# Performance work log

Measured on AMD Instinct MI355X. Metric: run time of the kernel, lower is better.

## Reference

```python
import jax, jax.numpy as jnp
import numpy as np

B, S, H = 4, 4096, 1024
E, K, DE, DS = 8, 2, 128, 512  # n_routed_experts, top_k, routed hidden, shared hidden


def setup_inputs() -> dict:
    key = jax.random.key(0)
    ks = jax.random.split(key, 10)
    sc = 0.02
    return {
        "x": jax.random.normal(ks[0], (B, S, H), dtype=jnp.float32),
        "Wg": jax.random.normal(ks[1], (E, H), dtype=jnp.float32) * sc,
        "W1": jax.random.normal(ks[2], (E, DE, H), dtype=jnp.float32) * sc,
        "b1": jnp.zeros((E, DE), dtype=jnp.float32),
        "W2": jax.random.normal(ks[3], (E, H, DE), dtype=jnp.float32) * sc,
        "b2": jnp.zeros((E, H), dtype=jnp.float32),
        "Ws1": jax.random.normal(ks[4], (DS, H), dtype=jnp.float32) * sc,
        "bs1": jnp.zeros((DS,), dtype=jnp.float32),
        "Ws2": jax.random.normal(ks[5], (H, DS), dtype=jnp.float32) * sc,
        "bs2": jnp.zeros((H,), dtype=jnp.float32),
    }


def reference(x, Wg, W1, b1, W2, b2, Ws1, bs1, Ws2, bs2):
    # FFNMoE forward, eval mode (dropout = identity, aux loss inactive).
    xf = x.reshape(-1, H)  # [T, H]
    # --- MOEGate: softmax scoring + top-k + normalized weights ---
    logits = xf @ Wg.T                         # [T, E]
    scores = jax.nn.softmax(logits, axis=-1)
    topk_w, topk_idx = jax.lax.top_k(scores, K)  # [T, K]
    topk_w = topk_w / (jnp.sum(topk_w, axis=-1, keepdims=True) + 1e-20)
    # Dense per-(token, expert) combine weight (topk indices are distinct).
    w = jnp.sum(jax.nn.one_hot(topk_idx, E, dtype=xf.dtype) * topk_w[..., None], axis=1)  # [T, E]
    # --- Routed experts: fc1 -> relu -> fc2, weighted scatter-combine ---
    h1 = jax.nn.relu(jnp.einsum('th,efh->tef', xf, W1) + b1)       # [T, E, DE]
    y = jnp.einsum('tef,ehf,te->th', h1, W2, w) + w @ b2           # [T, H]
    # --- Shared expert ---
    sh = jax.nn.relu(xf @ Ws1.T + bs1) @ Ws2.T + bs2               # [T, H]
    return (y + sh).reshape(x.shape)
```

## Files before the change

### kernel.cpp

```cpp
#include <hip/hip_runtime.h>
#include <cstdint>

#define TTOK 16384
#define HD   1024
#define NE   8
#define NDE  128
#define NDS  512
#define NC1  1536
#define KC2  1536
#define NPAIR 28
#define MAXT  160
#define PREPB 3080
#define GATEB 1024
#define NH    768

typedef float  f32x4  __attribute__((ext_vector_type(4)));
typedef __bf16 bf16x8 __attribute__((ext_vector_type(8)));

__device__ __forceinline__ unsigned short f2bf(float f) {
  unsigned int u = __float_as_uint(f);
  u += 0x7fffu + ((u >> 16) & 1u);
  return (unsigned short)(u >> 16);
}

__device__ __forceinline__ void gl2lds16(const void* gp, void* lp) {
  void* g0 = const_cast<void*>(gp);
  __builtin_amdgcn_global_load_lds((__attribute__((address_space(1))) void*)g0,
                                   (__attribute__((address_space(3))) void*)lp,
                                   16, 0, 0);
}

__global__ __launch_bounds__(256) void prep_gate(
    const float* __restrict__ x, const float* __restrict__ Wg,
    const float* __restrict__ W1, const float* __restrict__ Ws1,
    const float* __restrict__ W2, const float* __restrict__ Ws2,
    const float* __restrict__ b1, const float* __restrict__ bs1,
    unsigned short* __restrict__ W1cat, unsigned short* __restrict__ W2cat,
    float* __restrict__ bias1, unsigned short* __restrict__ xbf,
    float2* __restrict__ wpair, int* __restrict__ pid) {
  if (blockIdx.x < PREPB) {
    const int total = NC1 * HD + HD * KC2 + NC1;
    for (int idx = blockIdx.x * 256 + threadIdx.x; idx < total; idx += PREPB * 256) {
      if (idx < NC1 * HD) {
        int r = idx >> 10, k = idx & 1023;
        float v = (r < 1024) ? W1[idx] : Ws1[(size_t)(r - 1024) * HD + k];
        W1cat[idx] = f2bf(v);
      } else if (idx < NC1 * HD + HD * KC2) {
        int i2 = idx - NC1 * HD;
        int h = i2 / KC2;
        int j = i2 - h * KC2;
        float v = (j < 1024) ? W2[(size_t)((j >> 7) * HD + h) * NDE + (j & 127)]
                             : Ws2[(size_t)h * NDS + (j - 1024)];
        W2cat[i2] = f2bf(v);
      } else {
        int r = idx - (NC1 * HD + HD * KC2);
        bias1[r] = (r < 1024) ? b1[r] : bs1[r - 1024];
      }
    }
    return;
  }
  __shared__ float part[16 * 8 * 64];
  __shared__ float lgs[128];

  const int tid  = threadIdx.x;
  const int lane = tid & 63;
  const int wv   = tid >> 6;
  const int g    = blockIdx.x - PREPB;
  const int tokb = g * 16 + wv * 4;

  const float* xr = x + (size_t)tokb * HD + lane * 16;
  float4 xv[4][4];
#pragma unroll
  for (int t = 0; t < 4; ++t)
#pragma unroll
    for (int c = 0; c < 4; ++c)
      xv[t][c] = ((const float4*)(xr + (size_t)t * HD))[c];

#pragma unroll
  for (int t = 0; t < 4; ++t) {
    unsigned short* xo = xbf + (size_t)(tokb + t) * HD + lane * 16;
    union { unsigned short us[8]; uint4 v; } pk;
    pk.us[0] = f2bf(xv[t][0].x); pk.us[1] = f2bf(xv[t][0].y);
    pk.us[2] = f2bf(xv[t][0].z); pk.us[3] = f2bf(xv[t][0].w);
    pk.us[4] = f2bf(xv[t][1].x); pk.us[5] = f2bf(xv[t][1].y);
    pk.us[6] = f2bf(xv[t][1].z); pk.us[7] = f2bf(xv[t][1].w);
    ((uint4*)xo)[0] = pk.v;
    pk.us[0] = f2bf(xv[t][2].x); pk.us[1] = f2bf(xv[t][2].y);
    pk.us[2] = f2bf(xv[t][2].z); pk.us[3] = f2bf(xv[t][2].w);
    pk.us[4] = f2bf(xv[t][3].x); pk.us[5] = f2bf(xv[t][3].y);
    pk.us[6] = f2bf(xv[t][3].z); pk.us[7] = f2bf(xv[t][3].w);
    ((uint4*)xo)[1] = pk.v;
  }

  float p[4][8];
#pragma unroll
  for (int t = 0; t < 4; ++t)
#pragma unroll
    for (int e = 0; e < 8; ++e) p[t][e] = 0.f;
#pragma unroll
  for (int e = 0; e < 8; ++e) {
    const float4* wr = (const float4*)(Wg + (size_t)e * HD + lane * 16);
    float4 w0 = wr[0], w1 = wr[1], w2 = wr[2], w3 = wr[3];
#pragma unroll
    for (int t = 0; t < 4; ++t) {
      p[t][e] = w0.x * xv[t][0].x + w0.y * xv[t][0].y + w0.z * xv[t][0].z + w0.w * xv[t][0].w +
                w1.x * xv[t][1].x + w1.y * xv[t][1].y + w1.z * xv[t][1].z + w1.w * xv[t][1].w +
                w2.x * xv[t][2].x + w2.y * xv[t][2].y + w2.z * xv[t][2].z + w2.w * xv[t][2].w +
                w3.x * xv[t][3].x + w3.y * xv[t][3].y + w3.z * xv[t][3].z + w3.w * xv[t][3].w;
    }
  }
#pragma unroll
  for (int t = 0; t < 4; ++t)
#pragma unroll
    for (int e = 0; e < 8; ++e) {
      int j = (wv * 4 + t) * 8 + e;
      part[j * 64 + ((lane + 4 * j) & 63)] = p[t][e];
    }
  __syncthreads();

  if (tid < 128) {
    float s = 0.f;
#pragma unroll
    for (int m = 0; m < 16; ++m) {
      int kk = (4 * m + 4 * tid) & 63;
      float4 v = *(const float4*)&part[tid * 64 + kk];
      s += v.x + v.y + v.z + v.w;
    }
    lgs[tid] = s;
  }
  __syncthreads();

  if (tid < 16) {
    float lg[8];
#pragma unroll
    for (int e = 0; e < 8; ++e) lg[e] = lgs[tid * 8 + e];
    int i1 = 0; float m1 = lg[0];
#pragma unroll
    for (int e = 1; e < 8; ++e) { if (lg[e] > m1) { m1 = lg[e]; i1 = e; } }
    int i2 = -1; float m2 = -3.4e38f;
#pragma unroll
    for (int e = 0; e < 8; ++e) { if (e != i1 && lg[e] > m2) { m2 = lg[e]; i2 = e; } }
    float Z = 0.f;
#pragma unroll
    for (int e = 0; e < 8; ++e) Z += expf(lg[e] - m1);
    float s1 = 1.f / Z;
    float s2 = expf(m2 - m1) / Z;
    float dn = s1 + s2 + 1e-20f;
    float w1 = s1 / dn, w2 = s2 / dn;
    int ef, es; float wf, wsx;
    if (i1 < i2) { ef = i1; es = i2; wf = w1; wsx = w2; }
    else         { ef = i2; es = i1; wf = w2; wsx = w1; }
    int pq = ef * 7 - (ef * (ef - 1)) / 2 + (es - ef - 1);
    int t = g * 16 + tid;
    wpair[t] = make_float2(wf, wsx);
    pid[t] = pq;
  }
}

__global__ __launch_bounds__(256) void route_scan(const int* __restrict__ pid,
                                                  int* __restrict__ perm,
                                                  int4* __restrict__ tiletab,
                                                  int* __restrict__ ntct) {
  __shared__ int hist[256 * 29];
  __shared__ int totals[NPAIR];
  __shared__ int spre[256];
  const int p   = blockIdx.x;
  const int tid = threadIdx.x;
#pragma unroll
  for (int q = 0; q < 29; ++q) hist[tid * 29 + q] = 0;
  __syncthreads();
  for (int k = 0; k < 64; ++k) {
    int q = pid[tid + (k << 8)];
    hist[tid * 29 + q]++;
  }
  __syncthreads();
  if (tid < NPAIR) {
    int s = 0;
    for (int i = 0; i < 256; ++i) s += hist[i * 29 + tid];
    totals[tid] = s;
  }
  __syncthreads();
  const int mycnt = hist[tid * 29 + p];
  spre[tid] = mycnt;
  __syncthreads();
  for (int d = 1; d < 256; d <<= 1) {
    int add = (tid >= d) ? spre[tid - d] : 0;
    __syncthreads();
    spre[tid] += add;
    __syncthreads();
  }
  int estart = 0, tstart = 0;
  for (int q = 0; q < p; ++q) { estart += totals[q]; tstart += (totals[q] + 127) >> 7; }
  const int cp = totals[p];
  const int nt = (cp + 127) >> 7;
  if (p == NPAIR - 1 && tid == 0) ntct[0] = tstart + nt;
  for (int k = tid; k < nt; k += 256) {
    int4 e;
    e.x = p;
    e.y = estart + (k << 7);
    e.z = min(128, cp - (k << 7));
    e.w = (tstart + k) << 7;
    tiletab[tstart + k] = e;
  }
  int wr = estart + spre[tid] - mycnt;
  for (int k = 0; k < 64; ++k) {
    int t = tid + (k << 8);
    if (pid[t] == p) perm[wr++] = t;
  }
}

__global__ __launch_bounds__(256) void moe_fc1(const unsigned short* __restrict__ xbf,
                                               const unsigned short* __restrict__ W1cat,
                                               const int* __restrict__ perm,
                                               const float2* __restrict__ wpair,
                                               const float* __restrict__ bias1,
                                               const int4* __restrict__ tiletab,
                                               const int* __restrict__ ntct,
                                               unsigned short* __restrict__ Hbuf) {
  const int L   = blockIdx.x;
  const int xcd = L & 7;
  const int s   = L >> 3;
  const int mg  = s / 6;
  const int nn  = s - mg * 6;
  const int mt  = xcd + (mg << 3);
  if (mt >= ntct[0]) return;
  const int4 tt = tiletab[mt];
  const int eoff = tt.y, valid = tt.z, hbase = tt.w;
  int ef = 0, rem = tt.x;
  while (rem >= 7 - ef) { rem -= 7 - ef; ef++; }
  const int es = ef + 1 + rem;
  const int brow = (nn == 0) ? ef * 128 : (nn == 1) ? es * 128 : 1024 + ((nn - 2) << 7);

  __shared__ __align__(16) unsigned short As[128 * 64];
  __shared__ __align__(16) unsigned short Bs[128 * 64];

  const int tid  = threadIdx.x;
  const int lane = tid & 63;
  const int wv   = tid >> 6;
  const int wm   = wv >> 1;
  const int wn   = wv & 1;
  const int r16  = lane & 15;
  const int quad = lane >> 4;

  const unsigned short* gA[4];
  const unsigned short* gB[4];
  unsigned short* lA[4];
  unsigned short* lB[4];
#pragma unroll
  for (int i = 0; i < 4; ++i) {
    int idx = i * 256 + tid;
    int row = idx >> 3;
    int cc  = idx & 7;
    int kc  = cc ^ (row & 7);
    int tok = perm[eoff + min(row, valid - 1)];
    gA[i] = xbf + (size_t)tok * HD + kc * 8;
    gB[i] = W1cat + (size_t)(brow + row) * HD + kc * 8;
    lA[i] = As + idx * 8;
    lB[i] = Bs + idx * 8;
  }

  int aoff[4], boff[4];
#pragma unroll
  for (int i = 0; i < 4; ++i) {
    int ra = wm * 64 + i * 16 + r16;
    aoff[i] = ra * 64 + ((quad ^ (ra & 7)) << 3);
    int rb = wn * 64 + i * 16 + r16;
    boff[i] = rb * 64 + ((quad ^ (rb & 7)) << 3);
  }

  f32x4 acc[4][4];
#pragma unroll
  for (int i = 0; i < 4; ++i)
#pragma unroll
    for (int j = 0; j < 4; ++j) acc[i][j] = (f32x4){0.f, 0.f, 0.f, 0.f};

  for (int kt = 0; kt < 16; ++kt) {
    const int ko = kt << 6;
#pragma unroll
    for (int i = 0; i < 4; ++i) gl2lds16(gA[i] + ko, lA[i]);
#pragma unroll
    for (int i = 0; i < 4; ++i) gl2lds16(gB[i] + ko, lB[i]);
    __syncthreads();
#pragma unroll
    for (int g = 0; g < 2; ++g) {
      const int gx = g << 5;
      bf16x8 av[4], bv[4];
#pragma unroll
      for (int i = 0; i < 4; ++i) av[i] = *(const bf16x8*)(As + (aoff[i] ^ gx));
#pragma unroll
      for (int j = 0; j < 4; ++j) bv[j] = *(const bf16x8*)(Bs + (boff[j] ^ gx));
#pragma unroll
      for (int i = 0; i < 4; ++i)
#pragma unroll
        for (int j = 0; j < 4; ++j)
          acc[i][j] = __builtin_amdgcn_mfma_f32_16x16x32_bf16(av[i], bv[j], acc[i][j], 0, 0, 0);
    }
    __syncthreads();
  }

  float* wl = (float*)As;
  if (tid < 128) {
    int tok = perm[eoff + min(tid, valid - 1)];
    float sc = 1.0f;
    if (nn == 0) sc = wpair[tok].x;
    else if (nn == 1) sc = wpair[tok].y;
    wl[tid] = sc;
  }
  __syncthreads();
#pragma unroll
  for (int j = 0; j < 4; ++j) {
    const int cin = wn * 64 + j * 16 + r16;
    const float bz = bias1[brow + cin];
#pragma unroll
    for (int i = 0; i < 4; ++i) {
#pragma unroll
      for (int r = 0; r < 4; ++r) {
        const int lrow = wm * 64 + i * 16 + quad * 4 + r;
        float v = fmaxf(acc[i][j][r] + bz, 0.f) * wl[lrow];
        Hbuf[(size_t)(hbase + lrow) * NH + nn * 128 + cin] = f2bf(v);
      }
    }
  }
}

__global__ __launch_bounds__(256) void moe_fc2(const unsigned short* __restrict__ Hbuf,
                                               const unsigned short* __restrict__ W2cat,
                                               const int* __restrict__ perm,
                                               const float2* __restrict__ wpair,
                                               const float* __restrict__ b2,
                                               const float* __restrict__ bs2,
                                               const int4* __restrict__ tiletab,
                                               const int* __restrict__ ntct,
                                               float* __restrict__ out) {
  const int L   = blockIdx.x;
  const int xcd = L & 7;
  const int s   = L >> 3;
  const int mg  = s >> 3;
  const int nn  = s & 7;
  const int mt  = xcd + (mg << 3);
  if (mt >= ntct[0]) return;
  const int4 tt = tiletab[mt];
  const int eoff = tt.y, valid = tt.z, hbase = tt.w;
  int ef = 0, rem = tt.x;
  while (rem >= 7 - ef) { rem -= 7 - ef; ef++; }
  const int es = ef + 1 + rem;
  const int tileN = nn << 7;

  __shared__ __align__(16) unsigned short As[128 * 64];
  __shared__ __align__(16) unsigned short Bs[128 * 64];

  const int tid  = threadIdx.x;
  const int lane = tid & 63;
  const int wv   = tid >> 6;
  const int wm   = wv >> 1;
  const int wn   = wv & 1;
  const int r16  = lane & 15;
  const int quad = lane >> 4;

  const unsigned short* gA[4];
  const unsigned short* gB[4];
  unsigned short* lA[4];
  unsigned short* lB[4];
#pragma unroll
  for (int i = 0; i < 4; ++i) {
    int idx = i * 256 + tid;
    int row = idx >> 3;
    int cc  = idx & 7;
    int kc  = cc ^ (row & 7);
    gA[i] = Hbuf + (size_t)(hbase + row) * NH + kc * 8;
    gB[i] = W2cat + (size_t)(tileN + row) * KC2 + kc * 8;
    lA[i] = As + idx * 8;
    lB[i] = Bs + idx * 8;
  }

  int aoff[4], boff[4];
#pragma unroll
  for (int i = 0; i < 4; ++i) {
    int ra = wm * 64 + i * 16 + r16;
    aoff[i] = ra * 64 + ((quad ^ (ra & 7)) << 3);
    int rb = wn * 64 + i * 16 + r16;
    boff[i] = rb * 64 + ((quad ^ (rb & 7)) << 3);
  }

  f32x4 acc[4][4];
#pragma unroll
  for (int i = 0; i < 4; ++i)
#pragma unroll
    for (int j = 0; j < 4; ++j) acc[i][j] = (f32x4){0.f, 0.f, 0.f, 0.f};

  for (int kt = 0; kt < 12; ++kt) {
    const int koA = kt << 6;
    const int koB = (kt < 2) ? ef * 128 + (kt << 6)
                 : (kt < 4) ? es * 128 + ((kt - 2) << 6)
                            : 1024 + ((kt - 4) << 6);
#pragma unroll
    for (int i = 0; i < 4; ++i) gl2lds16(gA[i] + koA, lA[i]);
#pragma unroll
    for (int i = 0; i < 4; ++i) gl2lds16(gB[i] + koB, lB[i]);
    __syncthreads();
#pragma unroll
    for (int g = 0; g < 2; ++g) {
      const int gx = g << 5;
      bf16x8 av[4], bv[4];
#pragma unroll
      for (int i = 0; i < 4; ++i) av[i] = *(const bf16x8*)(As + (aoff[i] ^ gx));
#pragma unroll
      for (int j = 0; j < 4; ++j) bv[j] = *(const bf16x8*)(Bs + (boff[j] ^ gx));
#pragma unroll
      for (int i = 0; i < 4; ++i)
#pragma unroll
        for (int j = 0; j < 4; ++j)
          acc[i][j] = __builtin_amdgcn_mfma_f32_16x16x32_bf16(av[i], bv[j], acc[i][j], 0, 0, 0);
    }
    __syncthreads();
  }

  float2* wl2 = (float2*)As;
  int* tokl   = (int*)Bs;
  if (tid < 128) {
    int tokc = perm[eoff + min(tid, valid - 1)];
    tokl[tid] = (tid < valid) ? tokc : -1;
    wl2[tid] = wpair[tokc];
  }
  __syncthreads();
  float bsc[4], b2a[4], b2b[4];
#pragma unroll
  for (int j = 0; j < 4; ++j) {
    const int col = tileN + wn * 64 + j * 16 + r16;
    bsc[j] = bs2[col];
    b2a[j] = b2[(size_t)ef * HD + col];
    b2b[j] = b2[(size_t)es * HD + col];
  }
#pragma unroll
  for (int i = 0; i < 4; ++i) {
#pragma unroll
    for (int r = 0; r < 4; ++r) {
      const int lrow = wm * 64 + i * 16 + quad * 4 + r;
      const int tok = tokl[lrow];
      if (tok < 0) continue;
      const float2 w = wl2[lrow];
#pragma unroll
      for (int j = 0; j < 4; ++j) {
        const int col = tileN + wn * 64 + j * 16 + r16;
        out[(size_t)tok * HD + col] = acc[i][j][r] + bsc[j] + w.x * b2a[j] + w.y * b2b[j];
      }
    }
  }
}

extern "C" void kernel_launch(void* const* d_in, const int* in_sizes, int n_in,
                              void* d_out, int out_size, void* d_ws, size_t ws_size,
                              hipStream_t stream) {
  const float* x   = (const float*)d_in[0];
  const float* Wg  = (const float*)d_in[1];
  const float* W1  = (const float*)d_in[2];
  const float* b1  = (const float*)d_in[3];
  const float* W2  = (const float*)d_in[4];
  const float* b2  = (const float*)d_in[5];
  const float* Ws1 = (const float*)d_in[6];
  const float* bs1 = (const float*)d_in[7];
  const float* Ws2 = (const float*)d_in[8];
  const float* bs2 = (const float*)d_in[9];

  char* ws = (char*)d_ws;
  size_t off = 0;
  unsigned short* xbf   = (unsigned short*)(ws + off); off += (size_t)TTOK * HD * 2;
  unsigned short* Hbuf  = (unsigned short*)(ws + off); off += (size_t)MAXT * 128 * NH * 2;
  unsigned short* W1cat = (unsigned short*)(ws + off); off += (size_t)NC1 * HD * 2;
  unsigned short* W2cat = (unsigned short*)(ws + off); off += (size_t)HD * KC2 * 2;
  float* bias1          = (float*)(ws + off);          off += (size_t)NC1 * 4;
  float2* wpair         = (float2*)(ws + off);         off += (size_t)TTOK * 8;
  int* pid              = (int*)(ws + off);            off += (size_t)TTOK * 4;
  int* perm             = (int*)(ws + off);            off += (size_t)TTOK * 4;
  int4* tiletab         = (int4*)(ws + off);           off += (size_t)MAXT * 16;
  int* ntct             = (int*)(ws + off);            off += 16;

  prep_gate<<<PREPB + GATEB, 256, 0, stream>>>(x, Wg, W1, Ws1, W2, Ws2, b1, bs1,
                                               W1cat, W2cat, bias1, xbf, wpair, pid);
  route_scan<<<NPAIR, 256, 0, stream>>>(pid, perm, tiletab, ntct);
  moe_fc1<<<8 * 20 * 6, 256, 0, stream>>>(xbf, W1cat, perm, wpair, bias1, tiletab, ntct, Hbuf);
  moe_fc2<<<8 * 20 * 8, 256, 0, stream>>>(Hbuf, W2cat, perm, wpair, b2, bs2, tiletab, ntct,
                                          (float*)d_out);
}
```

Measured before the change: 250.1 us.

## Restructure expert GEMMs to one 128x128 tile per wave with double-buffered async loads

Both expert GEMM kernels now give each wavefront a whole 128x128 output tile, with private LDS double buffers filled by global_load_lds and vmcnt waits. This removes block-wide __syncthreads and overlaps the next K-slice load with the MFMA work, using smaller K steps of 32. The cost is a 256-register accumulator per wave and occupancy forced to one block per CU. Per-wave B-tile reuse is lost, and fewer blocks are launched.

```diff
diff --git a/kernel.cpp b/kernel.cpp
--- a/kernel.cpp
+++ b/kernel.cpp
@@ -29,6 +29,10 @@
                                    (__attribute__((address_space(3))) void*)lp,
                                    16, 0, 0);
 }
+
+#define VM16 asm volatile("s_waitcnt vmcnt(16)" ::: "memory")
+#define VM0  asm volatile("s_waitcnt vmcnt(0)"  ::: "memory")
+#define LGFENCE do { asm volatile("s_waitcnt lgkmcnt(0)" ::: "memory"); } while (0)
 
 __global__ __launch_bounds__(256) void prep_gate(
     const float* __restrict__ x, const float* __restrict__ Wg,
@@ -209,241 +213,212 @@
   }
 }
 
-__global__ __launch_bounds__(256) void moe_fc1(const unsigned short* __restrict__ xbf,
-                                               const unsigned short* __restrict__ W1cat,
-                                               const int* __restrict__ perm,
-                                               const float2* __restrict__ wpair,
-                                               const float* __restrict__ bias1,
-                                               const int4* __restrict__ tiletab,
-                                               const int* __restrict__ ntct,
-                                               unsigned short* __restrict__ Hbuf) {
-  const int L   = blockIdx.x;
-  const int xcd = L & 7;
-  const int s   = L >> 3;
-  const int mg  = s / 6;
-  const int nn  = s - mg * 6;
-  const int mt  = xcd + (mg << 3);
-  if (mt >= ntct[0]) return;
-  const int4 tt = tiletab[mt];
+__global__ __launch_bounds__(256, 1) void moe_fc1(
+    const unsigned short* __restrict__ xbf, const unsigned short* __restrict__ W1cat,
+    const int* __restrict__ perm, const float2* __restrict__ wpair,
+    const float* __restrict__ bias1, const int4* __restrict__ tiletab,
+    const int* __restrict__ ntct, unsigned short* __restrict__ Hbuf) {
+  __shared__ __align__(16) unsigned short lds[4][2][2][4096];
+  const int tid = threadIdx.x, lane = tid & 63, wv = tid >> 6;
+  const int job = blockIdx.x * 4 + wv;
+  const int tile = job / 6;
+  if (tile >= ntct[0]) return;
+  const int nn = job - tile * 6;
+  const int4 tt = tiletab[tile];
   const int eoff = tt.y, valid = tt.z, hbase = tt.w;
   int ef = 0, rem = tt.x;
   while (rem >= 7 - ef) { rem -= 7 - ef; ef++; }
   const int es = ef + 1 + rem;
-  const int brow = (nn == 0) ? ef * 128 : (nn == 1) ? es * 128 : 1024 + ((nn - 2) << 7);
-
-  __shared__ __align__(16) unsigned short As[128 * 64];
-  __shared__ __align__(16) unsigned short Bs[128 * 64];
-
-  const int tid  = threadIdx.x;
-  const int lane = tid & 63;
-  const int wv   = tid >> 6;
-  const int wm   = wv >> 1;
-  const int wn   = wv & 1;
-  const int r16  = lane & 15;
-  const int quad = lane >> 4;
-
-  const unsigned short* gA[4];
-  const unsigned short* gB[4];
-  unsigned short* lA[4];
-  unsigned short* lB[4];
-#pragma unroll
-  for (int i = 0; i < 4; ++i) {
-    int idx = i * 256 + tid;
-    int row = idx >> 3;
-    int cc  = idx & 7;
-    int kc  = cc ^ (row & 7);
-    int tok = perm[eoff + min(row, valid - 1)];
-    gA[i] = xbf + (size_t)tok * HD + kc * 8;
-    gB[i] = W1cat + (size_t)(brow + row) * HD + kc * 8;
-    lA[i] = As + idx * 8;
-    lB[i] = Bs + idx * 8;
-  }
-
-  int aoff[4], boff[4];
-#pragma unroll
-  for (int i = 0; i < 4; ++i) {
-    int ra = wm * 64 + i * 16 + r16;
-    aoff[i] = ra * 64 + ((quad ^ (ra & 7)) << 3);
-    int rb = wn * 64 + i * 16 + r16;
-    boff[i] = rb * 64 + ((quad ^ (rb & 7)) << 3);
-  }
-
-  f32x4 acc[4][4];
-#pragma unroll
-  for (int i = 0; i < 4; ++i)
-#pragma unroll
-    for (int j = 0; j < 4; ++j) acc[i][j] = (f32x4){0.f, 0.f, 0.f, 0.f};
-
-  for (int kt = 0; kt < 16; ++kt) {
-    const int ko = kt << 6;
-#pragma unroll
-    for (int i = 0; i < 4; ++i) gl2lds16(gA[i] + ko, lA[i]);
-#pragma unroll
-    for (int i = 0; i < 4; ++i) gl2lds16(gB[i] + ko, lB[i]);
-    __syncthreads();
-#pragma unroll
-    for (int g = 0; g < 2; ++g) {
-      const int gx = g << 5;
-      bf16x8 av[4], bv[4];
-#pragma unroll
-      for (int i = 0; i < 4; ++i) av[i] = *(const bf16x8*)(As + (aoff[i] ^ gx));
-#pragma unroll
-      for (int j = 0; j < 4; ++j) bv[j] = *(const bf16x8*)(Bs + (boff[j] ^ gx));
-#pragma unroll
-      for (int i = 0; i < 4; ++i)
-#pragma unroll
-        for (int j = 0; j < 4; ++j)
-          acc[i][j] = __builtin_amdgcn_mfma_f32_16x16x32_bf16(av[i], bv[j], acc[i][j], 0, 0, 0);
-    }
-    __syncthreads();
-  }
-
-  float* wl = (float*)As;
-  if (tid < 128) {
-    int tok = perm[eoff + min(tid, valid - 1)];
-    float sc = 1.0f;
-    if (nn == 0) sc = wpair[tok].x;
-    else if (nn == 1) sc = wpair[tok].y;
-    wl[tid] = sc;
-  }
-  __syncthreads();
-#pragma unroll
-  for (int j = 0; j < 4; ++j) {
-    const int cin = wn * 64 + j * 16 + r16;
-    const float bz = bias1[brow + cin];
-#pragma unroll
-    for (int i = 0; i < 4; ++i) {
-#pragma unroll
-      for (int r = 0; r < 4; ++r) {
-        const int lrow = wm * 64 + i * 16 + quad * 4 + r;
-        float v = fmaxf(acc[i][j][r] + bz, 0.f) * wl[lrow];
-        Hbuf[(size_t)(hbase + lrow) * NH + nn * 128 + cin] = f2bf(v);
+  const int brmap = (nn == 0) ? ef * 128 : (nn == 1) ? es * 128 : 1024 + ((nn - 2) << 7);
+
+  const int r16 = lane & 15, quad = lane >> 4;
+  const int kc8 = (lane & 3) ^ ((lane >> 3) & 3);
+  const int sw8 = (quad ^ ((r16 >> 1) & 3)) << 3;
+  int foff[8];
+#pragma unroll
+  for (int m = 0; m < 8; ++m) foff[m] = (m * 16 + r16) * 32 + sw8;
+
+  const unsigned short* gA[8];
+  const unsigned short* gB[8];
+#pragma unroll
+  for (int i = 0; i < 8; ++i) {
+    const int row = i * 16 + (lane >> 2);
+    const int tok = perm[eoff + min(row, valid - 1)];
+    gA[i] = xbf + (size_t)tok * HD + kc8 * 8;
+    gB[i] = W1cat + (size_t)(brmap + row) * HD + kc8 * 8;
+  }
+
+  f32x4 acc[8][8];
+#pragma unroll
+  for (int m = 0; m < 8; ++m)
+#pragma unroll
+    for (int n = 0; n < 8; ++n) acc[m][n] = (f32x4){0.f, 0.f, 0.f, 0.f};
+
+#define STG1(t, b) do { const int ko_ = (t) << 5;                                       \
+    unsigned short* la_ = &lds[wv][b][0][lane * 8];                                     \
+    unsigned short* lb_ = &lds[wv][b][1][lane * 8];                                     \
+    _Pragma("unroll") for (int i_ = 0; i_ < 8; ++i_) gl2lds16(gA[i_] + ko_, la_ + i_ * 512); \
+    _Pragma("unroll") for (int i_ = 0; i_ < 8; ++i_) gl2lds16(gB[i_] + ko_, lb_ + i_ * 512); } while (0)
+
+  STG1(0, 0);
+  STG1(1, 1);
+#pragma unroll 2
+  for (int t = 0; t < 32; ++t) {
+    if (t < 31) { VM16; } else { VM0; }
+    const int b = t & 1;
+    const unsigned short* Ab = &lds[wv][b][0][0];
+    const unsigned short* Bb = &lds[wv][b][1][0];
+    bf16x8 av[8], bv[8];
+#pragma unroll
+    for (int m = 0; m < 8; ++m) av[m] = *(const bf16x8*)(Ab + foff[m]);
+#pragma unroll
+    for (int n = 0; n < 8; ++n) bv[n] = *(const bf16x8*)(Bb + foff[n]);
+    __builtin_amdgcn_s_setprio(1);
+#pragma unroll
+    for (int m = 0; m < 8; ++m)
+#pragma unroll
+      for (int n = 0; n < 8; ++n)
+        acc[m][n] = __builtin_amdgcn_mfma_f32_16x16x32_bf16(av[m], bv[n], acc[m][n], 0, 0, 0);
+    __builtin_amdgcn_s_setprio(0);
+    if (t + 2 < 32) STG1(t + 2, b);
+  }
+#undef STG1
+
+  float* scl = (float*)&lds[wv][0][0][0];
+#pragma unroll
+  for (int rr = lane; rr < 128; rr += 64) {
+    const int tok = perm[eoff + min(rr, valid - 1)];
+    float s = 1.0f;
+    if (nn == 0) s = wpair[tok].x;
+    else if (nn == 1) s = wpair[tok].y;
+    scl[rr] = s;
+  }
+  LGFENCE;
+
+  float bz[8];
+#pragma unroll
+  for (int j = 0; j < 8; ++j) bz[j] = bias1[brmap + j * 16 + r16];
+#pragma unroll
+  for (int i = 0; i < 8; ++i) {
+#pragma unroll
+    for (int r = 0; r < 4; ++r) {
+      const int row = i * 16 + quad * 4 + r;
+      const float s = scl[row];
+      unsigned short* hp = Hbuf + (size_t)(hbase + row) * NH + nn * 128 + r16;
+#pragma unroll
+      for (int j = 0; j < 8; ++j) {
+        const float v = fmaxf(acc[i][j][r] + bz[j], 0.f) * s;
+        hp[j * 16] = f2bf(v);
       }
     }
   }
 }
 
-__global__ __launch_bounds__(256) void moe_fc2(const unsigned short* __restrict__ Hbuf,
-                                               const unsigned short* __restrict__ W2cat,
-                                               const int* __restrict__ perm,
-                                               const float2* __restrict__ wpair,
-                                               const float* __restrict__ b2,
-                                               const float* __restrict__ bs2,
-                                               const int4* __restrict__ tiletab,
-                                               const int* __restrict__ ntct,
-                                               float* __restrict__ out) {
-  const int L   = blockIdx.x;
-  const int xcd = L & 7;
-  const int s   = L >> 3;
-  const int mg  = s >> 3;
-  const int nn  = s & 7;
-  const int mt  = xcd + (mg << 3);
-  if (mt >= ntct[0]) return;
-  const int4 tt = tiletab[mt];
+__global__ __launch_bounds__(256, 1) void moe_fc2(
+    const unsigned short* __restrict__ Hbuf, const unsigned short* __restrict__ W2cat,
+    const int* __restrict__ perm, const float2* __restrict__ wpair,
+    const float* __restrict__ b2, const float* __restrict__ bs2,
+    const int4* __restrict__ tiletab, const int* __restrict__ ntct,
+    float* __restrict__ out) {
+  __shared__ __align__(16) unsigned short lds[4][2][2][4096];
+  const int tid = threadIdx.x, lane = tid & 63, wv = tid >> 6;
+  const int job = blockIdx.x * 4 + wv;
+  const int tile = job >> 3;
+  if (tile >= ntct[0]) return;
+  const int nn = job & 7;
+  const int4 tt = tiletab[tile];
   const int eoff = tt.y, valid = tt.z, hbase = tt.w;
   int ef = 0, rem = tt.x;
   while (rem >= 7 - ef) { rem -= 7 - ef; ef++; }
   const int es = ef + 1 + rem;
   const int tileN = nn << 7;
 
-  __shared__ __align__(16) unsigned short As[128 * 64];
-  __shared__ __align__(16) unsigned short Bs[128 * 64];
-
-  const int tid  = threadIdx.x;
-  const int lane = tid & 63;
-  const int wv   = tid >> 6;
-  const int wm   = wv >> 1;
-  const int wn   = wv & 1;
-  const int r16  = lane & 15;
-  const int quad = lane >> 4;
-
-  const unsigned short* gA[4];
-  const unsigned short* gB[4];
-  unsigned short* lA[4];
-  unsigned short* lB[4];
-#pragma unroll
-  for (int i = 0; i < 4; ++i) {
-    int idx = i * 256 + tid;
-    int row = idx >> 3;
-    int cc  = idx & 7;
-    int kc  = cc ^ (row & 7);
-    gA[i] = Hbuf + (size_t)(hbase + row) * NH + kc * 8;
-    gB[i] = W2cat + (size_t)(tileN + row) * KC2 + kc * 8;
-    lA[i] = As + idx * 8;
-    lB[i] = Bs + idx * 8;
-  }
-
-  int aoff[4], boff[4];
-#pragma unroll
-  for (int i = 0; i < 4; ++i) {
-    int ra = wm * 64 + i * 16 + r16;
-    aoff[i] = ra * 64 + ((quad ^ (ra & 7)) << 3);
-    int rb = wn * 64 + i * 16 + r16;
-    boff[i] = rb * 64 + ((quad ^ (rb & 7)) << 3);
-  }
-
-  f32x4 acc[4][4];
-#pragma unroll
-  for (int i = 0; i < 4; ++i)
-#pragma unroll
-    for (int j = 0; j < 4; ++j) acc[i][j] = (f32x4){0.f, 0.f, 0.f, 0.f};
-
-  for (int kt = 0; kt < 12; ++kt) {
-    const int koA = kt << 6;
-    const int koB = (kt < 2) ? ef * 128 + (kt << 6)
-                 : (kt < 4) ? es * 128 + ((kt - 2) << 6)
-                            : 1024 + ((kt - 4) << 6);
-#pragma unroll
-    for (int i = 0; i < 4; ++i) gl2lds16(gA[i] + koA, lA[i]);
-#pragma unroll
-    for (int i = 0; i < 4; ++i) gl2lds16(gB[i] + koB, lB[i]);
-    __syncthreads();
-#pragma unroll
-    for (int g = 0; g < 2; ++g) {
-      const int gx = g << 5;
-      bf16x8 av[4], bv[4];
-#pragma unroll
-      for (int i = 0; i < 4; ++i) av[i] = *(const bf16x8*)(As + (aoff[i] ^ gx));
-#pragma unroll
-      for (int j = 0; j < 4; ++j) bv[j] = *(const bf16x8*)(Bs + (boff[j] ^ gx));
-#pragma unroll
-      for (int i = 0; i < 4; ++i)
-#pragma unroll
-        for (int j = 0; j < 4; ++j)
-          acc[i][j] = __builtin_amdgcn_mfma_f32_16x16x32_bf16(av[i], bv[j], acc[i][j], 0, 0, 0);
-    }
-    __syncthreads();
-  }
-
-  float2* wl2 = (float2*)As;
-  int* tokl   = (int*)Bs;
-  if (tid < 128) {
-    int tokc = perm[eoff + min(tid, valid - 1)];
-    tokl[tid] = (tid < valid) ? tokc : -1;
-    wl2[tid] = wpair[tokc];
-  }
-  __syncthreads();
-  float bsc[4], b2a[4], b2b[4];
-#pragma unroll
-  for (int j = 0; j < 4; ++j) {
-    const int col = tileN + wn * 64 + j * 16 + r16;
+  const int r16 = lane & 15, quad = lane >> 4;
+  const int kc8 = (lane & 3) ^ ((lane >> 3) & 3);
+  const int sw8 = (quad ^ ((r16 >> 1) & 3)) << 3;
+  int foff[8];
+#pragma unroll
+  for (int m = 0; m < 8; ++m) foff[m] = (m * 16 + r16) * 32 + sw8;
+
+  const unsigned short* gA[8];
+  const unsigned short* gB[8];
+#pragma unroll
+  for (int i = 0; i < 8; ++i) {
+    const int row = i * 16 + (lane >> 2);
+    gA[i] = Hbuf + (size_t)(hbase + row) * NH + kc8 * 8;
+    gB[i] = W2cat + (size_t)(tileN + row) * KC2 + kc8 * 8;
+  }
+
+  f32x4 acc[8][8];
+#pragma unroll
+  for (int m = 0; m < 8; ++m)
+#pragma unroll
+    for (int n = 0; n < 8; ++n) acc[m][n] = (f32x4){0.f, 0.f, 0.f, 0.f};
+
+#define KOB2(t) ((t) < 4 ? ef * 128 + ((t) << 5)                      \
+               : (t) < 8 ? es * 128 + (((t) - 4) << 5)                \
+                         : 1024 + (((t) - 8) << 5))
+#define STG2(t, b) do { const int koA_ = (t) << 5; const int koB_ = KOB2(t);            \
+    unsigned short* la_ = &lds[wv][b][0][lane * 8];                                     \
+    unsigned short* lb_ = &lds[wv][b][1][lane * 8];                                     \
+    _Pragma("unroll") for (int i_ = 0; i_ < 8; ++i_) gl2lds16(gA[i_] + koA_, la_ + i_ * 512); \
+    _Pragma("unroll") for (int i_ = 0; i_ < 8; ++i_) gl2lds16(gB[i_] + koB_, lb_ + i_ * 512); } while (0)
+
+  STG2(0, 0);
+  STG2(1, 1);
+#pragma unroll 2
+  for (int t = 0; t < 24; ++t) {
+    if (t < 23) { VM16; } else { VM0; }
+    const int b = t & 1;
+    const unsigned short* Ab = &lds[wv][b][0][0];
+    const unsigned short* Bb = &lds[wv][b][1][0];
+    bf16x8 av[8], bv[8];
+#pragma unroll
+    for (int m = 0; m < 8; ++m) av[m] = *(const bf16x8*)(Ab + foff[m]);
+#pragma unroll
+    for (int n = 0; n < 8; ++n) bv[n] = *(const bf16x8*)(Bb + foff[n]);
+    __builtin_amdgcn_s_setprio(1);
+#pragma unroll
+    for (int m = 0; m < 8; ++m)
+#pragma unroll
+      for (int n = 0; n < 8; ++n)
+        acc[m][n] = __builtin_amdgcn_mfma_f32_16x16x32_bf16(av[m], bv[n], acc[m][n], 0, 0, 0);
+    __builtin_amdgcn_s_setprio(0);
+    if (t + 2 < 24) STG2(t + 2, b);
+  }
+#undef STG2
+#undef KOB2
+
+  int*    tkl = (int*)&lds[wv][0][0][0];
+  float2* wls = (float2*)&lds[wv][0][1][0];
+#pragma unroll
+  for (int rr = lane; rr < 128; rr += 64) {
+    const int tokc = perm[eoff + min(rr, valid - 1)];
+    tkl[rr] = (rr < valid) ? tokc : -1;
+    wls[rr] = wpair[tokc];
+  }
+  LGFENCE;
+
+  float bsc[8], b2a[8], b2b[8];
+#pragma unroll
+  for (int j = 0; j < 8; ++j) {
+    const int col = tileN + j * 16 + r16;
     bsc[j] = bs2[col];
     b2a[j] = b2[(size_t)ef * HD + col];
     b2b[j] = b2[(size_t)es * HD + col];
   }
 #pragma unroll
-  for (int i = 0; i < 4; ++i) {
+  for (int i = 0; i < 8; ++i) {
 #pragma unroll
     for (int r = 0; r < 4; ++r) {
-      const int lrow = wm * 64 + i * 16 + quad * 4 + r;
-      const int tok = tokl[lrow];
+      const int row = i * 16 + quad * 4 + r;
+      const int tok = tkl[row];
       if (tok < 0) continue;
-      const float2 w = wl2[lrow];
-#pragma unroll
-      for (int j = 0; j < 4; ++j) {
-        const int col = tileN + wn * 64 + j * 16 + r16;
-        out[(size_t)tok * HD + col] = acc[i][j][r] + bsc[j] + w.x * b2a[j] + w.y * b2b[j];
-      }
+      const float2 w = wls[row];
+      float* op = out + (size_t)tok * HD + tileN + r16;
+#pragma unroll
+      for (int j = 0; j < 8; ++j)
+        op[j * 16] = acc[i][j][r] + bsc[j] + w.x * b2a[j] + w.y * b2b[j];
     }
   }
 }
@@ -478,7 +453,8 @@
   prep_gate<<<PREPB + GATEB, 256, 0, stream>>>(x, Wg, W1, Ws1, W2, Ws2, b1, bs1,
                                                W1cat, W2cat, bias1, xbf, wpair, pid);
   route_scan<<<NPAIR, 256, 0, stream>>>(pid, perm, tiletab, ntct);
-  moe_fc1<<<8 * 20 * 6, 256, 0, stream>>>(xbf, W1cat, perm, wpair, bias1, tiletab, ntct, Hbuf);
-  moe_fc2<<<8 * 20 * 8, 256, 0, stream>>>(Hbuf, W2cat, perm, wpair, b2, bs2, tiletab, ntct,
-                                          (float*)d_out);
-}
+  moe_fc1<<<(MAXT * 6 + 3) / 4, 256, 0, stream>>>(xbf, W1cat, perm, wpair, bias1, tiletab, ntct,
+                                                  Hbuf);
+  moe_fc2<<<MAXT * 8 / 4, 256, 0, stream>>>(Hbuf, W2cat, perm, wpair, b2, bs2, tiletab, ntct,
+                                            (float*)d_out);
+}
```

New measurement: 488.4 us. 95.3% more time.

## Replace per-pair histogram scan with atomic ranking plus prefix and fill kernels

Applied to the files above, without the earlier changes.

Token-to-expert-pair routing used to be a 28-block kernel where each block rebuilt a full histogram and rescanned all 16384 tokens. Now the gate step takes a per-pair slot with an atomic counter. A tiny single-block kernel then computes pair offsets and the tile table, and a fully parallel kernel scatters each token into the permutation. This removes serial scan work on a few blocks, at the cost of an extra memset, an extra launch, and nondeterministic token order within each pair.

```diff
diff --git a/kernel.cpp b/kernel.cpp
--- a/kernel.cpp
+++ b/kernel.cpp
@@ -37,7 +37,8 @@
     const float* __restrict__ b1, const float* __restrict__ bs1,
     unsigned short* __restrict__ W1cat, unsigned short* __restrict__ W2cat,
     float* __restrict__ bias1, unsigned short* __restrict__ xbf,
-    float2* __restrict__ wpair, int* __restrict__ pid) {
+    float2* __restrict__ wpair, int* __restrict__ pid,
+    int* __restrict__ pcur, int* __restrict__ prank) {
   if (blockIdx.x < PREPB) {
     const int total = NC1 * HD + HD * KC2 + NC1;
     for (int idx = blockIdx.x * 256 + threadIdx.x; idx < total; idx += PREPB * 256) {
@@ -154,59 +155,50 @@
     int t = g * 16 + tid;
     wpair[t] = make_float2(wf, wsx);
     pid[t] = pq;
-  }
-}
-
-__global__ __launch_bounds__(256) void route_scan(const int* __restrict__ pid,
-                                                  int* __restrict__ perm,
-                                                  int4* __restrict__ tiletab,
-                                                  int* __restrict__ ntct) {
-  __shared__ int hist[256 * 29];
-  __shared__ int totals[NPAIR];
-  __shared__ int spre[256];
-  const int p   = blockIdx.x;
+    prank[t] = atomicAdd(&pcur[pq], 1);
+  }
+}
+
+__global__ __launch_bounds__(64) void route_prefix(const int* __restrict__ pcur,
+                                                   int4* __restrict__ tiletab,
+                                                   int* __restrict__ ntct,
+                                                   int* __restrict__ est) {
+  __shared__ int tot[NPAIR];
+  __shared__ int eoffs[NPAIR], toffs[NPAIR], ntt[NPAIR];
   const int tid = threadIdx.x;
-#pragma unroll
-  for (int q = 0; q < 29; ++q) hist[tid * 29 + q] = 0;
-  __syncthreads();
-  for (int k = 0; k < 64; ++k) {
-    int q = pid[tid + (k << 8)];
-    hist[tid * 29 + q]++;
-  }
-  __syncthreads();
-  if (tid < NPAIR) {
-    int s = 0;
-    for (int i = 0; i < 256; ++i) s += hist[i * 29 + tid];
-    totals[tid] = s;
-  }
-  __syncthreads();
-  const int mycnt = hist[tid * 29 + p];
-  spre[tid] = mycnt;
-  __syncthreads();
-  for (int d = 1; d < 256; d <<= 1) {
-    int add = (tid >= d) ? spre[tid - d] : 0;
-    __syncthreads();
-    spre[tid] += add;
-    __syncthreads();
-  }
-  int estart = 0, tstart = 0;
-  for (int q = 0; q < p; ++q) { estart += totals[q]; tstart += (totals[q] + 127) >> 7; }
-  const int cp = totals[p];
-  const int nt = (cp + 127) >> 7;
-  if (p == NPAIR - 1 && tid == 0) ntct[0] = tstart + nt;
-  for (int k = tid; k < nt; k += 256) {
-    int4 e;
-    e.x = p;
-    e.y = estart + (k << 7);
-    e.z = min(128, cp - (k << 7));
-    e.w = (tstart + k) << 7;
-    tiletab[tstart + k] = e;
-  }
-  int wr = estart + spre[tid] - mycnt;
-  for (int k = 0; k < 64; ++k) {
-    int t = tid + (k << 8);
-    if (pid[t] == p) perm[wr++] = t;
-  }
+  if (tid < NPAIR) tot[tid] = pcur[tid];
+  __syncthreads();
+  if (tid == 0) {
+    int e = 0, ts = 0;
+    for (int p = 0; p < NPAIR; ++p) {
+      const int c = tot[p];
+      eoffs[p] = e; toffs[p] = ts; ntt[p] = (c + 127) >> 7;
+      est[p] = e;
+      e += c; ts += ntt[p];
+    }
+    ntct[0] = ts;
+  }
+  __syncthreads();
+  for (int p = 0; p < NPAIR; ++p) {
+    const int nt = ntt[p];
+    for (int k = tid; k < nt; k += 64) {
+      int4 en;
+      en.x = p;
+      en.y = eoffs[p] + (k << 7);
+      en.z = min(128, tot[p] - (k << 7));
+      en.w = (toffs[p] + k) << 7;
+      tiletab[toffs[p] + k] = en;
+    }
+  }
+}
+
+__global__ __launch_bounds__(256) void route_fill(const int* __restrict__ pid,
+                                                  const int* __restrict__ prank,
+                                                  const int* __restrict__ est,
+                                                  int* __restrict__ perm) {
+  const int t = blockIdx.x * 256 + threadIdx.x;
+  const int q = pid[t];
+  perm[est[q] + prank[t]] = t;
 }
 
 __global__ __launch_bounds__(256) void moe_fc1(const unsigned short* __restrict__ xbf,
@@ -472,12 +464,18 @@
   float2* wpair         = (float2*)(ws + off);         off += (size_t)TTOK * 8;
   int* pid              = (int*)(ws + off);            off += (size_t)TTOK * 4;
   int* perm             = (int*)(ws + off);            off += (size_t)TTOK * 4;
+  int* prank            = (int*)(ws + off);            off += (size_t)TTOK * 4;
   int4* tiletab         = (int4*)(ws + off);           off += (size_t)MAXT * 16;
   int* ntct             = (int*)(ws + off);            off += 16;
-
+  int* pcur             = (int*)(ws + off);            off += (size_t)NPAIR * 4;
+  int* est              = (int*)(ws + off);            off += (size_t)NPAIR * 4;
+
+  hipMemsetAsync(pcur, 0, NPAIR * sizeof(int), stream);
   prep_gate<<<PREPB + GATEB, 256, 0, stream>>>(x, Wg, W1, Ws1, W2, Ws2, b1, bs1,
-                                               W1cat, W2cat, bias1, xbf, wpair, pid);
-  route_scan<<<NPAIR, 256, 0, stream>>>(pid, perm, tiletab, ntct);
+                                               W1cat, W2cat, bias1, xbf, wpair, pid,
+                                               pcur, prank);
+  route_prefix<<<1, 64, 0, stream>>>(pcur, tiletab, ntct, est);
+  route_fill<<<TTOK / 256, 256, 0, stream>>>(pid, prank, est, perm);
   moe_fc1<<<8 * 20 * 6, 256, 0, stream>>>(xbf, W1cat, perm, wpair, bias1, tiletab, ntct, Hbuf);
   moe_fc2<<<8 * 20 * 8, 256, 0, stream>>>(Hbuf, W2cat, perm, wpair, b2, bs2, tiletab, ntct,
                                           (float*)d_out);
```

Result: slower. 268.5 us (+7.4%).
